# Kernel tuning notes

Measured on AMD Instinct MI355X. Metric: run time of the kernel, lower is better.

The kernel has to match this reference:

```python
import jax, jax.numpy as jnp
import numpy as np

ML_R_PRIORI = 1.5   # mainlobe_window_radius_priori
ML_R_MAX = 4        # mainlobe_window_radius_max
MIN_K = 1           # min_k
ML_WIDTH_POW = 1    # ml_width_pow
DIST_SENTINEL = 100.0


def _grid_offsets(r):
    # all (dy, dx) pairs in [-r, r]^2 -> [(2r+1)^2, 2]
    o = np.arange(-r, r + 1)
    yy, xx = np.meshgrid(o, o, indexing='ij')
    return np.stack([yy.ravel(), xx.ravel()], axis=-1).astype(np.int32)


def setup_inputs() -> dict:
    key = jax.random.key(0)
    B, C, H, W = 256, 324, 18, 18
    k1, k2 = jax.random.split(key)
    cost_volume = jax.random.normal(k1, (B, C, H, W), dtype=jnp.float32)
    peak_coords = jax.random.randint(k2, (B, C, 2), 0, H, dtype=jnp.int32)  # (y, x)
    gy, gx = jnp.meshgrid(jnp.arange(H, dtype=jnp.int32),
                          jnp.arange(W, dtype=jnp.int32), indexing='ij')
    mesh_y = jnp.broadcast_to(gy, (B, C, H, W))
    mesh_x = jnp.broadcast_to(gx, (B, C, H, W))
    return {"cost_volume": cost_volume, "peak_coords": peak_coords,
            "mesh_y": mesh_y, "mesh_x": mesh_x}


def reference(cost_volume, peak_coords, mesh_y, mesh_x):
    B, C, H, W = cost_volume.shape
    BC, HW = B * C, H * W
    cv = cost_volume.reshape(BC, HW)
    peak = peak_coords.reshape(BC, 2)
    my = mesh_y.reshape(BC, HW)
    mx = mesh_x.reshape(BC, HW)

    # --- static offset tables ---
    off_max = jnp.asarray(_grid_offsets(ML_R_MAX))                     # [81, 2]
    off_p = jnp.asarray(_grid_offsets(int(np.ceil(ML_R_PRIORI))))      # [25, 2]
    norm_p = jnp.sqrt(jnp.sum(off_p.astype(jnp.float32) ** 2, -1))
    off_priori = jnp.where((norm_p <= ML_R_PRIORI)[:, None], off_p, 0)  # out-of-radius -> (0,0)

    bidx = jnp.arange(BC)[:, None]

    def scatter_zero_mask(offsets):
        # offsets: [1 or BC, N, 2]; zero out mainlobe window around each peak
        win = peak[:, None, :] + offsets
        wy = jnp.clip(win[..., 0], 0, H - 1)
        wx = jnp.clip(win[..., 1], 0, W - 1)
        flat = wy * W + wx                                  # [BC, N]
        return jnp.ones((BC, HW), jnp.float32).at[bidx, flat].set(0.0)

    # --- priori sidelobe mean ---
    w_pri = scatter_zero_mask(off_priori[None])
    n_pri = w_pri.sum(-1, keepdims=True)
    mean_pri = (cv * w_pri).sum(-1, keepdims=True) / n_pri

    # --- distance to nearest below-mean (sidelobe) point -> mainlobe width ---
    py, px = peak[:, :1], peak[:, 1:]
    dist = jnp.sqrt(((my - py) ** 2 + (mx - px) ** 2).astype(jnp.float32))
    pos = jnp.arange(HW, dtype=jnp.int32)[None]
    peak_flat = py * W + px
    keep = (cv <= mean_pri) & (pos != peak_flat)
    dist = jnp.where(keep, dist, DIST_SENTINEL)
    neg_small, _ = jax.lax.top_k(-dist, MIN_K)              # k smallest distances
    width = (-neg_small).mean(-1, keepdims=True)            # [BC, 1]

    # --- data-dependent mainlobe window (per-row radius) ---
    radius = jnp.clip(width, 1.5, ML_R_MAX + 0.5)           # [BC, 1]
    norms_max = jnp.sqrt(jnp.sum(off_max.astype(jnp.float32) ** 2, -1))  # [81]
    in_r = norms_max[None, :] <= radius                     # [BC, 81]
    off_dyn = jnp.where(in_r[..., None], off_max[None], 0)  # [BC, 81, 2]

    w = scatter_zero_mask(off_dyn)
    n = w.sum(-1, keepdims=True)
    mean_s = (cv * w).sum(-1, keepdims=True) / n
    var_s = (((cv - mean_s) * w) ** 2).sum(-1, keepdims=True) / (n - 1.0)  # use_std_dev=False
    peaks = cv.max(-1, keepdims=True)

    psrw = ((peaks - mean_s) / (var_s * width ** ML_WIDTH_POW + 1e-16)).reshape(B, C)
    saliency = psrw / (psrw.mean(-1, keepdims=True) + 1e-8)
    return saliency
```

## Files before the change

### kernel.cpp

```cpp
#include <hip/hip_runtime.h>
#include <math.h>

constexpr int Hn = 18, Wn = 18, HWn = 324;

template<int N>
__device__ __forceinline__ float ror16_f(float x) {
    return __int_as_float(__builtin_amdgcn_mov_dpp(
        __float_as_int(x), 0x120 | N, 0xF, 0xF, true));
}
template<int N>
__device__ __forceinline__ unsigned ror16_u(unsigned x) {
    return (unsigned)__builtin_amdgcn_mov_dpp(
        (int)x, 0x120 | N, 0xF, 0xF, true);
}
template<int N>
__device__ __forceinline__ int ror16_i(int x) {
    return __builtin_amdgcn_mov_dpp(x, 0x120 | N, 0xF, 0xF, true);
}

__global__ __launch_bounds__(256, 6) void psrw_kernel(
    const float* __restrict__ cv, const int* __restrict__ peak,
    float* __restrict__ out, int BC)
{
    int gtid = blockIdx.x * 256 + threadIdx.x;
    int wave = gtid >> 6;
    int lane = threadIdx.x & 63;
    int g = lane >> 4;
    int l = lane & 15;
    int tile = wave * 4 + g;
    if (tile >= BC) return;

    const float* row = cv + (size_t)tile * HWn;
    int2 pk = ((const int2*)peak)[tile];
    int py = pk.x & 31, px = pk.y & 31;

    const float* colp = row + l;
    float c[21];
#pragma unroll
    for (int j = 0; j < 18; ++j) c[j] = colp[18 * j];
    int lh = l >> 1, lb = l & 1;
    const float* tp = row + (lh * 18 + 16 + lb);
    c[18] = tp[0];
    c[19] = tp[144];
    bool v20 = (l < 4);
    c[20] = v20 ? tp[288] : 0.f;

    float cpk = row[py * Wn + px];

    float m0 = -INFINITY, m1 = -INFINITY, s0 = 0.f, s1 = 0.f;
#pragma unroll
    for (int j = 0; j < 18; j += 2) { m0 = fmaxf(m0, c[j]); s0 += c[j]; }
#pragma unroll
    for (int j = 1; j < 18; j += 2) { m1 = fmaxf(m1, c[j]); s1 += c[j]; }
    m0 = fmaxf(m0, c[18]); s0 += c[18];
    m1 = fmaxf(m1, c[19]); s1 += c[19];
    m0 = fmaxf(m0, v20 ? c[20] : -INFINITY); s0 += c[20];
    float m = fmaxf(m0, m1);
    float s = s0 + s1;

    int ry0 = max(0, py - 1), ry1 = min(Hn - 1, py + 1);
    int rx0 = max(0, px - 1), rx1 = min(Wn - 1, px + 1);
    float rectc = 0.f;
    if (l < 9) {
        int q = (l * 11) >> 5;
        int r = l - 3 * q;
        int ry = ry0 + q, rx = rx0 + r;
        if (ry <= ry1 && rx <= rx1) rectc = row[ry * Wn + rx];
    }
    s -= rectc;
    s += ror16_f<8>(s);  m = fmaxf(m, ror16_f<8>(m));
    s += ror16_f<4>(s);  m = fmaxf(m, ror16_f<4>(m));
    s += ror16_f<2>(s);  m = fmaxf(m, ror16_f<2>(m));
    s += ror16_f<1>(s);  m = fmaxf(m, ror16_f<1>(m));
    int n_pri = HWn - (ry1 - ry0 + 1) * (rx1 - rx0 + 1);
    float mean_pri = s / (float)n_pri;

    int dxl = l - px;
    int dx2m1 = dxl * dxl - 1;
    unsigned A = (unsigned)(py * py + dx2m1);
    int Bs = 1 - 2 * py;
    unsigned dminb = 0xFFFFFFFFu;
#pragma unroll
    for (int j = 0; j < 18; ++j) {
        unsigned t = min(dminb, A);
        dminb = (c[j] <= mean_pri) ? t : dminb;
        A += (unsigned)Bs; Bs += 2;
    }
    int dyt = lh - py;
    int dxt = 16 + lb - px;
    int dxt2m1 = dxt * dxt - 1;
#pragma unroll
    for (int s2 = 0; s2 < 3; ++s2) {
        int dy = dyt + 8 * s2;
        unsigned dd = (unsigned)(dy * dy + dxt2m1);
        if (s2 == 2 && !v20) dd = 0x7FFFFFFFu;
        unsigned t = min(dminb, dd);
        dminb = (c[18 + s2] <= mean_pri) ? t : dminb;
    }
    dminb = min(dminb, ror16_u<8>(dminb));
    dminb = min(dminb, ror16_u<4>(dminb));
    dminb = min(dminb, ror16_u<2>(dminb));
    dminb = min(dminb, ror16_u<1>(dminb));

    float width = (dminb > 577u) ? 100.f
                                 : __builtin_amdgcn_sqrtf((float)(dminb + 1u));
    unsigned rad2m1 = min(max(dminb, 1u), 19u);

    float sd0 = 0.f, sd1 = 0.f, ssd = 0.f;
    int cnt = 0;
    unsigned A2 = (unsigned)(py * py + dx2m1);
    int Bs2 = 1 - 2 * py;
#pragma unroll
    for (int j = 0; j < 18; ++j) {
        bool in = (A2 <= rad2m1);
        float cm = in ? 0.f : c[j];
        if (j & 1) sd1 += cm; else sd0 += cm;
        ssd = fmaf(cm, cm, ssd);
        cnt += in ? 1 : 0;
        A2 += (unsigned)Bs2; Bs2 += 2;
    }
#pragma unroll
    for (int s2 = 0; s2 < 3; ++s2) {
        int dy = dyt + 8 * s2;
        unsigned dd = (unsigned)(dy * dy + dxt2m1);
        if (s2 == 2 && !v20) dd = 0x7FFFFFFFu;
        bool in = (dd <= rad2m1);
        float cm = in ? 0.f : c[18 + s2];
        if (s2 & 1) sd1 += cm; else sd0 += cm;
        ssd = fmaf(cm, cm, ssd);
        cnt += in ? 1 : 0;
    }
    float sd = sd0 + sd1;
    sd += ror16_f<8>(sd);  ssd += ror16_f<8>(ssd);  cnt += ror16_i<8>(cnt);
    sd += ror16_f<4>(sd);  ssd += ror16_f<4>(ssd);  cnt += ror16_i<4>(cnt);
    sd += ror16_f<2>(sd);  ssd += ror16_f<2>(ssd);  cnt += ror16_i<2>(cnt);
    sd += ror16_f<1>(sd);  ssd += ror16_f<1>(ssd);  cnt += ror16_i<1>(cnt);
    sd -= cpk;
    ssd = fmaf(-cpk, cpk, ssd);
    float n = (float)(HWn - 1 - cnt);
    float mean_s = sd * __builtin_amdgcn_rcpf(n);
    float var_s = fmaf(-sd, mean_s, ssd) * __builtin_amdgcn_rcpf(n - 1.f);
    float psrw = (m - mean_s) * __builtin_amdgcn_rcpf(fmaf(var_s, width, 1e-16f));
    if (l == 0) out[tile] = psrw;
}

__global__ __launch_bounds__(256) void norm_kernel(float* __restrict__ out, int B)
{
    int gtid = blockIdx.x * 256 + threadIdx.x;
    int wave = gtid >> 6;
    int lane = threadIdx.x & 63;
    if (wave >= B) return;
    float* row = out + (size_t)wave * HWn;
    float4 v0 = reinterpret_cast<float4*>(row)[lane];
    bool has2 = lane < 17;
    float4 v1 = make_float4(0.f, 0.f, 0.f, 0.f);
    if (has2) v1 = reinterpret_cast<float4*>(row)[64 + lane];
    float s = (v0.x + v0.y) + (v0.z + v0.w) + ((v1.x + v1.y) + (v1.z + v1.w));
#pragma unroll
    for (int o = 32; o; o >>= 1) s += __shfl_xor(s, o, 64);
    float denom = s / 324.0f + 1e-8f;
    v0.x /= denom; v0.y /= denom; v0.z /= denom; v0.w /= denom;
    reinterpret_cast<float4*>(row)[lane] = v0;
    if (has2) {
        v1.x /= denom; v1.y /= denom; v1.z /= denom; v1.w /= denom;
        reinterpret_cast<float4*>(row)[64 + lane] = v1;
    }
}

extern "C" void kernel_launch(void* const* d_in, const int* in_sizes, int n_in,
                              void* d_out, int out_size, void* d_ws, size_t ws_size,
                              hipStream_t stream) {
    const float* cv  = (const float*)d_in[0];
    const int* peak  = (const int*)d_in[1];
    float* out = (float*)d_out;

    int BC = in_sizes[1] / 2;
    int waves = (BC + 3) / 4;
    int blocks1 = (waves + 3) / 4;
    psrw_kernel<<<blocks1, 256, 0, stream>>>(cv, peak, out, BC);

    int B = out_size / HWn;
    int blocks2 = (B + 3) / 4;
    norm_kernel<<<blocks2, 256, 0, stream>>>(out, B);
}
```

Before: 25.20 us.

## Compute sidelobe stats by subtracting a 9x9 peak window from full-row sums

The full-row sum of squares is now accumulated in the first pass over the row. The dynamic-radius window stats are obtained from a 9x9 window gathered around the peak, with 9 loads per lane, and subtracted from the totals instead of making a second masked pass over all 21 elements. This trades the second full pass for 9 extra global loads per lane plus extra DPP reductions. Subtracting from totals (computing E[x^2] minus the masked part) can cost floating-point accuracy. The occupancy hint in launch_bounds is also removed.

```diff
diff --git a/kernel.cpp b/kernel.cpp
--- a/kernel.cpp
+++ b/kernel.cpp
@@ -18,7 +18,7 @@
     return __builtin_amdgcn_mov_dpp(x, 0x120 | N, 0xF, 0xF, true);
 }
 
-__global__ __launch_bounds__(256, 6) void psrw_kernel(
+__global__ __launch_bounds__(256) void psrw_kernel(
     const float* __restrict__ cv, const int* __restrict__ peak,
     float* __restrict__ out, int BC)
 {
@@ -47,33 +47,55 @@
 
     float cpk = row[py * Wn + px];
 
-    float m0 = -INFINITY, m1 = -INFINITY, s0 = 0.f, s1 = 0.f;
+    int ox = l - 4;
+    int xraw = px + ox;
+    int xs = min(max(xraw, 0), 17);
+    bool xv = ((unsigned)xraw < 18u);
+    int ystart = min(max(py - 4, 0), 9);
+    const float* wbase = row + ystart * 18 + xs;
+    float wv[9];
 #pragma unroll
-    for (int j = 0; j < 18; j += 2) { m0 = fmaxf(m0, c[j]); s0 += c[j]; }
+    for (int k = 0; k < 9; ++k) wv[k] = wbase[18 * k];
+    int ox2m1 = ox * ox - 1;
+    int dyb = ystart - py;
+
+    float m0 = -INFINITY, m1 = -INFINITY, s0 = 0.f, s1 = 0.f, q0 = 0.f, q1 = 0.f;
 #pragma unroll
-    for (int j = 1; j < 18; j += 2) { m1 = fmaxf(m1, c[j]); s1 += c[j]; }
-    m0 = fmaxf(m0, c[18]); s0 += c[18];
-    m1 = fmaxf(m1, c[19]); s1 += c[19];
-    m0 = fmaxf(m0, v20 ? c[20] : -INFINITY); s0 += c[20];
+    for (int j = 0; j < 18; j += 2) {
+        m0 = fmaxf(m0, c[j]); s0 += c[j]; q0 = fmaf(c[j], c[j], q0);
+    }
+#pragma unroll
+    for (int j = 1; j < 18; j += 2) {
+        m1 = fmaxf(m1, c[j]); s1 += c[j]; q1 = fmaf(c[j], c[j], q1);
+    }
+    m0 = fmaxf(m0, c[18]); s0 += c[18]; q0 = fmaf(c[18], c[18], q0);
+    m1 = fmaxf(m1, c[19]); s1 += c[19]; q1 = fmaf(c[19], c[19], q1);
+    m0 = fmaxf(m0, v20 ? c[20] : -INFINITY); s0 += c[20]; q0 = fmaf(c[20], c[20], q0);
     float m = fmaxf(m0, m1);
     float s = s0 + s1;
+    float q = q0 + q1;
 
     int ry0 = max(0, py - 1), ry1 = min(Hn - 1, py + 1);
     int rx0 = max(0, px - 1), rx1 = min(Wn - 1, px + 1);
     float rectc = 0.f;
     if (l < 9) {
-        int q = (l * 11) >> 5;
-        int r = l - 3 * q;
-        int ry = ry0 + q, rx = rx0 + r;
+        int qd = (l * 11) >> 5;
+        int r = l - 3 * qd;
+        int ry = ry0 + qd, rx = rx0 + r;
         if (ry <= ry1 && rx <= rx1) rectc = row[ry * Wn + rx];
     }
-    s -= rectc;
-    s += ror16_f<8>(s);  m = fmaxf(m, ror16_f<8>(m));
-    s += ror16_f<4>(s);  m = fmaxf(m, ror16_f<4>(m));
-    s += ror16_f<2>(s);  m = fmaxf(m, ror16_f<2>(m));
-    s += ror16_f<1>(s);  m = fmaxf(m, ror16_f<1>(m));
+    float sm = s - rectc;
+    sm += ror16_f<8>(sm); m = fmaxf(m, ror16_f<8>(m));
+    q  += ror16_f<8>(q);  rectc += ror16_f<8>(rectc);
+    sm += ror16_f<4>(sm); m = fmaxf(m, ror16_f<4>(m));
+    q  += ror16_f<4>(q);  rectc += ror16_f<4>(rectc);
+    sm += ror16_f<2>(sm); m = fmaxf(m, ror16_f<2>(m));
+    q  += ror16_f<2>(q);  rectc += ror16_f<2>(rectc);
+    sm += ror16_f<1>(sm); m = fmaxf(m, ror16_f<1>(m));
+    q  += ror16_f<1>(q);  rectc += ror16_f<1>(rectc);
     int n_pri = HWn - (ry1 - ry0 + 1) * (rx1 - rx0 + 1);
-    float mean_pri = s / (float)n_pri;
+    float mean_pri = sm / (float)n_pri;
+    float s_total = sm + rectc;
 
     int dxl = l - px;
     int dx2m1 = dxl * dxl - 1;
@@ -106,38 +128,26 @@
                                  : __builtin_amdgcn_sqrtf((float)(dminb + 1u));
     unsigned rad2m1 = min(max(dminb, 1u), 19u);
 
-    float sd0 = 0.f, sd1 = 0.f, ssd = 0.f;
-    int cnt = 0;
-    unsigned A2 = (unsigned)(py * py + dx2m1);
-    int Bs2 = 1 - 2 * py;
+    float ds = 0.f, dss = 0.f;
+    int dcnt = 0;
 #pragma unroll
-    for (int j = 0; j < 18; ++j) {
-        bool in = (A2 <= rad2m1);
-        float cm = in ? 0.f : c[j];
-        if (j & 1) sd1 += cm; else sd0 += cm;
-        ssd = fmaf(cm, cm, ssd);
-        cnt += in ? 1 : 0;
-        A2 += (unsigned)Bs2; Bs2 += 2;
+    for (int k = 0; k < 9; ++k) {
+        int oy = dyb + k;
+        unsigned d2m1 = (unsigned)(oy * oy + ox2m1);
+        bool val = (d2m1 <= rad2m1) & xv;
+        float cm = val ? wv[k] : 0.f;
+        ds += cm;
+        dss = fmaf(cm, cm, dss);
+        dcnt += val ? 1 : 0;
     }
-#pragma unroll
-    for (int s2 = 0; s2 < 3; ++s2) {
-        int dy = dyt + 8 * s2;
-        unsigned dd = (unsigned)(dy * dy + dxt2m1);
-        if (s2 == 2 && !v20) dd = 0x7FFFFFFFu;
-        bool in = (dd <= rad2m1);
-        float cm = in ? 0.f : c[18 + s2];
-        if (s2 & 1) sd1 += cm; else sd0 += cm;
-        ssd = fmaf(cm, cm, ssd);
-        cnt += in ? 1 : 0;
-    }
-    float sd = sd0 + sd1;
-    sd += ror16_f<8>(sd);  ssd += ror16_f<8>(ssd);  cnt += ror16_i<8>(cnt);
-    sd += ror16_f<4>(sd);  ssd += ror16_f<4>(ssd);  cnt += ror16_i<4>(cnt);
-    sd += ror16_f<2>(sd);  ssd += ror16_f<2>(ssd);  cnt += ror16_i<2>(cnt);
-    sd += ror16_f<1>(sd);  ssd += ror16_f<1>(ssd);  cnt += ror16_i<1>(cnt);
-    sd -= cpk;
-    ssd = fmaf(-cpk, cpk, ssd);
-    float n = (float)(HWn - 1 - cnt);
+    ds += ror16_f<8>(ds); dss += ror16_f<8>(dss); dcnt += ror16_i<8>(dcnt);
+    ds += ror16_f<4>(ds); dss += ror16_f<4>(dss); dcnt += ror16_i<4>(dcnt);
+    ds += ror16_f<2>(ds); dss += ror16_f<2>(dss); dcnt += ror16_i<2>(dcnt);
+    ds += ror16_f<1>(ds); dss += ror16_f<1>(dss); dcnt += ror16_i<1>(dcnt);
+
+    float sd = s_total - ds - cpk;
+    float ssd = fmaf(-cpk, cpk, q - dss);
+    float n = (float)(HWn - 1 - dcnt);
     float mean_s = sd * __builtin_amdgcn_rcpf(n);
     float var_s = fmaf(-sd, mean_s, ssd) * __builtin_amdgcn_rcpf(n - 1.f);
     float psrw = (m - mean_s) * __builtin_amdgcn_rcpf(fmaf(var_s, width, 1e-16f));
```

Result: no change. 25.30 us (+0.4%).
